# Kernel optimization log

Measured on AMD Instinct MI355X. Metric: run time of the kernel, lower is better.

## Reference

```python
import jax, jax.numpy as jnp
import numpy as np

B, P, E, D, A = 128, 196, 2048, 512, 512


def setup_inputs() -> dict:
    key = jax.random.key(0)
    ks = jax.random.split(key, 8)
    s = lambda fan_in: 1.0 / np.sqrt(fan_in)
    return {
        "encoder_out": jax.random.normal(ks[0], (B, P, E), jnp.float32),
        "decoder_hidden": jax.random.normal(ks[1], (B, D), jnp.float32),
        "We": jax.random.uniform(ks[2], (E, A), jnp.float32, -s(E), s(E)),
        "be": jax.random.uniform(ks[3], (A,), jnp.float32, -s(E), s(E)),
        "Wd": jax.random.uniform(ks[4], (D, A), jnp.float32, -s(D), s(D)),
        "bd": jax.random.uniform(ks[5], (A,), jnp.float32, -s(D), s(D)),
        "Wf": jax.random.uniform(ks[6], (A, 1), jnp.float32, -s(A), s(A)),
        "bf": jax.random.uniform(ks[7], (1,), jnp.float32, -s(A), s(A)),
    }


def reference(encoder_out, decoder_hidden, We, be, Wd, bd, Wf, bf):
    # att1: [B, P, A]
    att1 = jnp.einsum("bpe,ea->bpa", encoder_out, We) + be
    # att2: [B, A]
    att2 = decoder_hidden @ Wd + bd
    # additive attention scores: [B, P]
    att = (jax.nn.relu(att1 + att2[:, None, :]) @ Wf + bf)[..., 0]
    alpha = jax.nn.softmax(att, axis=1)  # softmax over pixels
    # weighted sum over pixels: [B, E]
    awe = jnp.einsum("bpe,bp->be", encoder_out, alpha)
    return awe, alpha
```

## Files before the change

kernel.cpp:

```cpp
#include <hip/hip_runtime.h>
#include <hip/hip_bf16.h>

typedef __attribute__((ext_vector_type(4))) float f32x4;
typedef __attribute__((ext_vector_type(4))) unsigned int u32x4;
typedef __attribute__((ext_vector_type(8))) short s16x8;

#define B_  128
#define P_  196
#define E_  2048
#define D_  512
#define A_  512
#define M_  (B_*P_)

typedef __attribute__((address_space(1))) const unsigned int gu32;
typedef __attribute__((address_space(3))) unsigned int lu32;
__device__ __forceinline__ void gl_lds16(const void* g, void* l) {
  __builtin_amdgcn_global_load_lds((gu32*)g, (lu32*)l, 16, 0, 0);
}

#define WAIT_VM6() asm volatile("s_waitcnt vmcnt(6)" ::: "memory")
#define WAIT_VM0() asm volatile("s_waitcnt vmcnt(0)" ::: "memory")
#define WAIT_LGKM0() asm volatile("s_waitcnt lgkmcnt(0)" ::: "memory")

__global__ void we_conv_kernel(const float* __restrict__ We,
                               unsigned short* __restrict__ WeTs) {
  __shared__ float tile[32][33];
  const int tx = threadIdx.x, ty = threadIdx.y;
  const int a0 = blockIdx.x * 32, e0 = blockIdx.y * 32;
  tile[ty][tx] = We[(e0 + ty) * A_ + a0 + tx];
  __syncthreads();
  const float v = tile[tx][ty];
  const unsigned int u = __float_as_uint(v);
  const unsigned short r = (unsigned short)((u + 0x7fffu + ((u >> 16) & 1u)) >> 16);
  const int a = a0 + ty;
  const int kt = blockIdx.y;
  const int c8 = tx >> 3, j = tx & 7;
  const int dest = ((a * 32 + c8 * 8) ^ ((a & 7) << 3)) + j;
  WeTs[kt * 16384 + dest] = r;
}

__global__ void att2_kernel(const float* __restrict__ h, const float* __restrict__ Wd,
                            const float* __restrict__ bd, const float* __restrict__ be,
                            float* __restrict__ att2pb) {
  const int b = blockIdx.x;
  const int t = threadIdx.x;
  __shared__ float hs[D_];
  hs[t] = h[b * D_ + t];
  hs[t + 256] = h[b * D_ + t + 256];
  __syncthreads();
  float a0 = 0.f, a1 = 0.f;
  for (int d = 0; d < D_; ++d) {
    const float hv = hs[d];
    a0 = fmaf(hv, Wd[d * A_ + t], a0);
    a1 = fmaf(hv, Wd[d * A_ + t + 256], a1);
  }
  att2pb[b * A_ + t] = a0 + bd[t] + be[t];
  att2pb[b * A_ + t + 256] = a1 + bd[t + 256] + be[t + 256];
}

__device__ inline unsigned pk2(float a, float b) {
  union { __hip_bfloat162 h; unsigned u; } cv;
  cv.h = __float22bfloat162_rn(make_float2(a, b));
  return cv.u;
}
__device__ inline u32x4 cvt8(const f32x4 lo, const f32x4 hi) {
  u32x4 r;
  r[0] = pk2(lo[0], lo[1]);
  r[1] = pk2(lo[2], lo[3]);
  r[2] = pk2(hi[0], hi[1]);
  r[3] = pk2(hi[2], hi[3]);
  return r;
}

__launch_bounds__(512, 2)
__global__ void score_kernel(const float* __restrict__ enc,
                             const unsigned short* __restrict__ WeTs,
                             const float* __restrict__ att2pb,
                             const float* __restrict__ Wf,
                             float* __restrict__ att_part) {
  __shared__ unsigned short Bh[3][512 * 32];
  __shared__ unsigned short Ahs[3][128 * 32];

  const int bid = blockIdx.x;
  const int m0 = bid * 128;

  const int t = threadIdx.x;
  const int lane = t & 63, w = t >> 6;
  const int wm = (w >> 2) * 64;
  const int wn = (w & 3) * 128;

  const int ar = t >> 2, ac = t & 3;
  const float* aptr = enc + (size_t)(m0 + ar) * E_ + ac * 8;
  const int awz = (ar * 32 + ac * 8) ^ ((ar & 7) << 3);
  const int doff = t * 8;

  const int q = lane >> 4, fr = lane & 15;
  const int fx = (fr & 7) << 3;
  int fa[4], fb[8];
#pragma unroll
  for (int i = 0; i < 4; ++i) fa[i] = ((wm + i * 16 + fr) * 32 + q * 8) ^ fx;
#pragma unroll
  for (int j = 0; j < 8; ++j) fb[j] = ((wn + j * 16 + fr) * 32 + q * 8) ^ fx;

  const f32x4 zero = {0.f, 0.f, 0.f, 0.f};
  f32x4 acc[4][8];
#pragma unroll
  for (int mi = 0; mi < 4; ++mi)
#pragma unroll
    for (int ni = 0; ni < 8; ++ni) acc[mi][ni] = zero;

  unsigned short *bAc = &Ahs[0][0], *bA1 = &Ahs[1][0], *bA2 = &Ahs[2][0];
  unsigned short *bBc = &Bh[0][0],  *bB1 = &Bh[1][0],  *bB2 = &Bh[2][0];

  f32x4 aC0, aC1, aN0, aN1;

  {
    aC0 = *(const f32x4*)(aptr);
    aC1 = *(const f32x4*)(aptr + 4);
#pragma unroll
    for (int i = 0; i < 4; ++i)
      gl_lds16(WeTs + i * 4096 + doff, bBc + i * 4096 + doff);
    aN0 = *(const f32x4*)(aptr + 32);
    aN1 = *(const f32x4*)(aptr + 36);
#pragma unroll
    for (int i = 0; i < 4; ++i)
      gl_lds16(WeTs + 16384 + i * 4096 + doff, bB1 + i * 4096 + doff);
    const u32x4 av = cvt8(aC0, aC1);
    *(u32x4*)(bAc + awz) = av;
    aC0 = aN0; aC1 = aN1;
    WAIT_VM6();
    WAIT_LGKM0();
    __builtin_amdgcn_s_barrier();
  }

  for (int it = 0; it < 62; ++it) {
    const int kof = (it + 2) * 32;
    aN0 = *(const f32x4*)(aptr + kof);
    aN1 = *(const f32x4*)(aptr + kof + 4);
    const unsigned short* srcB = WeTs + (size_t)(it + 2) * 16384;
#pragma unroll
    for (int i = 0; i < 4; ++i)
      gl_lds16(srcB + i * 4096 + doff, bB2 + i * 4096 + doff);

    s16x8 fah[4], fbh[8];
#pragma unroll
    for (int j = 0; j < 8; ++j) fbh[j] = *(const s16x8*)(bBc + fb[j]);
#pragma unroll
    for (int i = 0; i < 4; ++i) fah[i] = *(const s16x8*)(bAc + fa[i]);
    __builtin_amdgcn_s_setprio(1);
#pragma unroll
    for (int mi = 0; mi < 4; ++mi)
#pragma unroll
      for (int ni = 0; ni < 8; ++ni)
        acc[mi][ni] = __builtin_amdgcn_mfma_f32_16x16x32_bf16(fah[mi], fbh[ni], acc[mi][ni], 0, 0, 0);
    __builtin_amdgcn_s_setprio(0);

    {
      const u32x4 av = cvt8(aC0, aC1);
      *(u32x4*)(bA1 + awz) = av;
    }
    aC0 = aN0; aC1 = aN1;

    WAIT_VM6();
    WAIT_LGKM0();
    __builtin_amdgcn_s_barrier();

    unsigned short* tmp;
    tmp = bAc; bAc = bA1; bA1 = bA2; bA2 = tmp;
    tmp = bBc; bBc = bB1; bB1 = bB2; bB2 = tmp;
  }

  {
    s16x8 fah[4], fbh[8];
#pragma unroll
    for (int j = 0; j < 8; ++j) fbh[j] = *(const s16x8*)(bBc + fb[j]);
#pragma unroll
    for (int i = 0; i < 4; ++i) fah[i] = *(const s16x8*)(bAc + fa[i]);
    __builtin_amdgcn_s_setprio(1);
#pragma unroll
    for (int mi = 0; mi < 4; ++mi)
#pragma unroll
      for (int ni = 0; ni < 8; ++ni)
        acc[mi][ni] = __builtin_amdgcn_mfma_f32_16x16x32_bf16(fah[mi], fbh[ni], acc[mi][ni], 0, 0, 0);
    __builtin_amdgcn_s_setprio(0);
    const u32x4 av = cvt8(aC0, aC1);
    *(u32x4*)(bA1 + awz) = av;
    WAIT_VM0();
    WAIT_LGKM0();
    __builtin_amdgcn_s_barrier();
  }

  {
    s16x8 fah[4], fbh[8];
#pragma unroll
    for (int j = 0; j < 8; ++j) fbh[j] = *(const s16x8*)(bB1 + fb[j]);
#pragma unroll
    for (int i = 0; i < 4; ++i) fah[i] = *(const s16x8*)(bA1 + fa[i]);
#pragma unroll
    for (int mi = 0; mi < 4; ++mi)
#pragma unroll
      for (int ni = 0; ni < 8; ++ni)
        acc[mi][ni] = __builtin_amdgcn_mfma_f32_16x16x32_bf16(fah[mi], fbh[ni], acc[mi][ni], 0, 0, 0);
  }

  const int colL = wn + fr;
  float wfv[8];
#pragma unroll
  for (int ni = 0; ni < 8; ++ni) wfv[ni] = Wf[colL + ni * 16];
#pragma unroll
  for (int mi = 0; mi < 4; ++mi) {
    const int rowb = m0 + wm + mi * 16 + (q << 2);
#pragma unroll
    for (int r = 0; r < 4; ++r) {
      const int row = rowb + r;
      const int bb = row / P_;
      const float* a2 = att2pb + bb * A_ + colL;
      float s = 0.f;
#pragma unroll
      for (int ni = 0; ni < 8; ++ni)
        s += fmaxf(acc[mi][ni][r] + a2[ni * 16], 0.f) * wfv[ni];
#pragma unroll
      for (int off = 1; off < 16; off <<= 1) s += __shfl_xor(s, off);
      if (fr == 0) att_part[row * 4 + (w & 3)] = s;
    }
  }
}

__global__ void softmax_awe_kernel(const float* __restrict__ enc,
                                   const float* __restrict__ att_part,
                                   float* __restrict__ out) {
  const int bid = blockIdx.x;
  const int b = bid >> 1, ch = bid & 1;
  const int t = threadIdx.x;
  __shared__ float sm[256];
  __shared__ float alpha_s[P_];

  float av = -1e30f;
  if (t < P_) {
    const float* apt = att_part + (b * P_ + t) * 4;
    av = (apt[0] + apt[1]) + (apt[2] + apt[3]);
  }
  sm[t] = av;
  __syncthreads();
  for (int st = 128; st > 0; st >>= 1) {
    if (t < st) sm[t] = fmaxf(sm[t], sm[t + st]);
    __syncthreads();
  }
  const float mx = sm[0];
  __syncthreads();
  float ev = 0.f;
  if (t < P_) ev = __expf(av - mx);
  sm[t] = ev;
  __syncthreads();
  for (int st = 128; st > 0; st >>= 1) {
    if (t < st) sm[t] += sm[t + st];
    __syncthreads();
  }
  const float denom = sm[0];
  const float al = ev / denom;
  if (t < P_) {
    alpha_s[t] = al;
    if (ch == 0) out[B_ * E_ + b * P_ + t] = al;
  }
  __syncthreads();

  const int e0 = ch * 1024 + t * 4;
  const float* ebase = enc + (size_t)b * P_ * E_ + e0;
  f32x4 acc = {0.f, 0.f, 0.f, 0.f};
  for (int p = 0; p < P_; ++p) {
    const f32x4 v = *(const f32x4*)(ebase + (size_t)p * E_);
    const float a = alpha_s[p];
    acc.x += a * v.x; acc.y += a * v.y; acc.z += a * v.z; acc.w += a * v.w;
  }
  *(f32x4*)(out + b * E_ + e0) = acc;
}

extern "C" void kernel_launch(void* const* d_in, const int* in_sizes, int n_in,
                              void* d_out, int out_size, void* d_ws, size_t ws_size,
                              hipStream_t stream) {
  const float* enc = (const float*)d_in[0];
  const float* h   = (const float*)d_in[1];
  const float* We  = (const float*)d_in[2];
  const float* be  = (const float*)d_in[3];
  const float* Wd  = (const float*)d_in[4];
  const float* bd  = (const float*)d_in[5];
  const float* Wf  = (const float*)d_in[6];
  float* out = (float*)d_out;

  float* att2pb = (float*)d_ws;
  float* att_part = att2pb + B_ * A_;
  unsigned short* WeTs = (unsigned short*)(att_part + M_ * 4);

  we_conv_kernel<<<dim3(A_ / 32, E_ / 32), dim3(32, 32), 0, stream>>>(We, WeTs);
  att2_kernel<<<B_, 256, 0, stream>>>(h, Wd, bd, be, att2pb);
  score_kernel<<<M_ / 128, 512, 0, stream>>>(enc, WeTs, att2pb, Wf, att_part);
  softmax_awe_kernel<<<B_ * 2, 256, 0, stream>>>(enc, att_part, out);
}
```

Before: 133.7 us.

## Split score GEMM N dimension into 128-wide tiles with XCD-aware block remap

The score GEMM changes from 128x512 tiles on 512-thread blocks to 128x128 tiles on 256-thread blocks. This gives four times as many blocks and smaller LDS and accumulator use per block, with three blocks per CU. The block index is remapped so that consecutive blocks on the same XCD share M rows, meant to improve L2 reuse of the encoder rows. The cost is that each encoder tile is loaded and converted to bf16 four times instead of once, and the attention partial sums widen to eight per row, which the softmax kernel must now reduce. The weight pre-layout is adjusted to match the per-N-block tiles.

```diff
diff --git a/kernel.cpp b/kernel.cpp
--- a/kernel.cpp
+++ b/kernel.cpp
@@ -34,9 +34,10 @@
   const unsigned short r = (unsigned short)((u + 0x7fffu + ((u >> 16) & 1u)) >> 16);
   const int a = a0 + ty;
   const int kt = blockIdx.y;
+  const int nb = a >> 7, al = a & 127;
   const int c8 = tx >> 3, j = tx & 7;
-  const int dest = ((a * 32 + c8 * 8) ^ ((a & 7) << 3)) + j;
-  WeTs[kt * 16384 + dest] = r;
+  const int dest = ((al * 32 + c8 * 8) ^ ((al & 7) << 3)) + j;
+  WeTs[(kt * 4 + nb) * 4096 + dest] = r;
 }
 
 __global__ void att2_kernel(const float* __restrict__ h, const float* __restrict__ Wd,
@@ -72,62 +73,72 @@
   return r;
 }
 
-__launch_bounds__(512, 2)
+__launch_bounds__(256, 3)
 __global__ void score_kernel(const float* __restrict__ enc,
                              const unsigned short* __restrict__ WeTs,
                              const float* __restrict__ att2pb,
                              const float* __restrict__ Wf,
                              float* __restrict__ att_part) {
-  __shared__ unsigned short Bh[3][512 * 32];
-  __shared__ unsigned short Ahs[3][128 * 32];
-
-  const int bid = blockIdx.x;
-  const int m0 = bid * 128;
+  __shared__ unsigned short Ahs[3][4096];
+  __shared__ unsigned short Bhs[3][4096];
+
+  const int orig = blockIdx.x;
+  const int bid = (orig & 7) * 98 + (orig >> 3);
+  const int mb = bid >> 2, nb = bid & 3;
+  const int m0 = mb * 128;
+  const int n0 = nb * 128;
 
   const int t = threadIdx.x;
   const int lane = t & 63, w = t >> 6;
-  const int wm = (w >> 2) * 64;
-  const int wn = (w & 3) * 128;
+  const int wm = (w >> 1) * 64;
+  const int wn = (w & 1) * 64;
 
   const int ar = t >> 2, ac = t & 3;
   const float* aptr = enc + (size_t)(m0 + ar) * E_ + ac * 8;
-  const int awz = (ar * 32 + ac * 8) ^ ((ar & 7) << 3);
+  const int awz0 = (ar * 32 + ac * 8) ^ ((ar & 7) << 3);
+  const int awz1 = ((ar + 64) * 32 + ac * 8) ^ ((ar & 7) << 3);
+
+  const unsigned short* bsrc = WeTs + (size_t)nb * 4096;
   const int doff = t * 8;
 
   const int q = lane >> 4, fr = lane & 15;
   const int fx = (fr & 7) << 3;
-  int fa[4], fb[8];
-#pragma unroll
-  for (int i = 0; i < 4; ++i) fa[i] = ((wm + i * 16 + fr) * 32 + q * 8) ^ fx;
-#pragma unroll
-  for (int j = 0; j < 8; ++j) fb[j] = ((wn + j * 16 + fr) * 32 + q * 8) ^ fx;
+  int fa[4], fb[4];
+#pragma unroll
+  for (int i = 0; i < 4; ++i) {
+    fa[i] = ((wm + i * 16 + fr) * 32 + q * 8) ^ fx;
+    fb[i] = ((wn + i * 16 + fr) * 32 + q * 8) ^ fx;
+  }
 
   const f32x4 zero = {0.f, 0.f, 0.f, 0.f};
-  f32x4 acc[4][8];
+  f32x4 acc[4][4];
 #pragma unroll
   for (int mi = 0; mi < 4; ++mi)
 #pragma unroll
-    for (int ni = 0; ni < 8; ++ni) acc[mi][ni] = zero;
+    for (int ni = 0; ni < 4; ++ni) acc[mi][ni] = zero;
 
   unsigned short *bAc = &Ahs[0][0], *bA1 = &Ahs[1][0], *bA2 = &Ahs[2][0];
-  unsigned short *bBc = &Bh[0][0],  *bB1 = &Bh[1][0],  *bB2 = &Bh[2][0];
-
-  f32x4 aC0, aC1, aN0, aN1;
+  unsigned short *bBc = &Bhs[0][0], *bB1 = &Bhs[1][0], *bB2 = &Bhs[2][0];
+
+  f32x4 aC[4], aN[4];
 
   {
-    aC0 = *(const f32x4*)(aptr);
-    aC1 = *(const f32x4*)(aptr + 4);
-#pragma unroll
-    for (int i = 0; i < 4; ++i)
-      gl_lds16(WeTs + i * 4096 + doff, bBc + i * 4096 + doff);
-    aN0 = *(const f32x4*)(aptr + 32);
-    aN1 = *(const f32x4*)(aptr + 36);
-#pragma unroll
-    for (int i = 0; i < 4; ++i)
-      gl_lds16(WeTs + 16384 + i * 4096 + doff, bB1 + i * 4096 + doff);
-    const u32x4 av = cvt8(aC0, aC1);
-    *(u32x4*)(bAc + awz) = av;
-    aC0 = aN0; aC1 = aN1;
+    aC[0] = *(const f32x4*)(aptr);
+    aC[1] = *(const f32x4*)(aptr + 4);
+    aC[2] = *(const f32x4*)(aptr + 64 * E_);
+    aC[3] = *(const f32x4*)(aptr + 64 * E_ + 4);
+    gl_lds16(bsrc + doff, bBc + doff);
+    gl_lds16(bsrc + 2048 + doff, bBc + 2048 + doff);
+    aN[0] = *(const f32x4*)(aptr + 32);
+    aN[1] = *(const f32x4*)(aptr + 36);
+    aN[2] = *(const f32x4*)(aptr + 64 * E_ + 32);
+    aN[3] = *(const f32x4*)(aptr + 64 * E_ + 36);
+    gl_lds16(bsrc + 16384 + doff, bB1 + doff);
+    gl_lds16(bsrc + 16384 + 2048 + doff, bB1 + 2048 + doff);
+    *(u32x4*)(bAc + awz0) = cvt8(aC[0], aC[1]);
+    *(u32x4*)(bAc + awz1) = cvt8(aC[2], aC[3]);
+#pragma unroll
+    for (int i = 0; i < 4; ++i) aC[i] = aN[i];
     WAIT_VM6();
     WAIT_LGKM0();
     __builtin_amdgcn_s_barrier();
@@ -135,31 +146,32 @@
 
   for (int it = 0; it < 62; ++it) {
     const int kof = (it + 2) * 32;
-    aN0 = *(const f32x4*)(aptr + kof);
-    aN1 = *(const f32x4*)(aptr + kof + 4);
-    const unsigned short* srcB = WeTs + (size_t)(it + 2) * 16384;
-#pragma unroll
-    for (int i = 0; i < 4; ++i)
-      gl_lds16(srcB + i * 4096 + doff, bB2 + i * 4096 + doff);
-
-    s16x8 fah[4], fbh[8];
-#pragma unroll
-    for (int j = 0; j < 8; ++j) fbh[j] = *(const s16x8*)(bBc + fb[j]);
-#pragma unroll
-    for (int i = 0; i < 4; ++i) fah[i] = *(const s16x8*)(bAc + fa[i]);
+    aN[0] = *(const f32x4*)(aptr + kof);
+    aN[1] = *(const f32x4*)(aptr + kof + 4);
+    aN[2] = *(const f32x4*)(aptr + kof + 64 * E_);
+    aN[3] = *(const f32x4*)(aptr + kof + 64 * E_ + 4);
+    const unsigned short* sb = bsrc + (size_t)(it + 2) * 16384;
+    gl_lds16(sb + doff, bB2 + doff);
+    gl_lds16(sb + 2048 + doff, bB2 + 2048 + doff);
+
+    s16x8 fah[4], fbh[4];
+#pragma unroll
+    for (int i = 0; i < 4; ++i) {
+      fah[i] = *(const s16x8*)(bAc + fa[i]);
+      fbh[i] = *(const s16x8*)(bBc + fb[i]);
+    }
     __builtin_amdgcn_s_setprio(1);
 #pragma unroll
     for (int mi = 0; mi < 4; ++mi)
 #pragma unroll
-      for (int ni = 0; ni < 8; ++ni)
+      for (int ni = 0; ni < 4; ++ni)
         acc[mi][ni] = __builtin_amdgcn_mfma_f32_16x16x32_bf16(fah[mi], fbh[ni], acc[mi][ni], 0, 0, 0);
     __builtin_amdgcn_s_setprio(0);
 
-    {
-      const u32x4 av = cvt8(aC0, aC1);
-      *(u32x4*)(bA1 + awz) = av;
-    }
-    aC0 = aN0; aC1 = aN1;
+    *(u32x4*)(bA1 + awz0) = cvt8(aC[0], aC[1]);
+    *(u32x4*)(bA1 + awz1) = cvt8(aC[2], aC[3]);
+#pragma unroll
+    for (int i = 0; i < 4; ++i) aC[i] = aN[i];
 
     WAIT_VM6();
     WAIT_LGKM0();
@@ -171,42 +183,44 @@
   }
 
   {
-    s16x8 fah[4], fbh[8];
-#pragma unroll
-    for (int j = 0; j < 8; ++j) fbh[j] = *(const s16x8*)(bBc + fb[j]);
-#pragma unroll
-    for (int i = 0; i < 4; ++i) fah[i] = *(const s16x8*)(bAc + fa[i]);
+    s16x8 fah[4], fbh[4];
+#pragma unroll
+    for (int i = 0; i < 4; ++i) {
+      fah[i] = *(const s16x8*)(bAc + fa[i]);
+      fbh[i] = *(const s16x8*)(bBc + fb[i]);
+    }
     __builtin_amdgcn_s_setprio(1);
 #pragma unroll
     for (int mi = 0; mi < 4; ++mi)
 #pragma unroll
-      for (int ni = 0; ni < 8; ++ni)
+      for (int ni = 0; ni < 4; ++ni)
         acc[mi][ni] = __builtin_amdgcn_mfma_f32_16x16x32_bf16(fah[mi], fbh[ni], acc[mi][ni], 0, 0, 0);
     __builtin_amdgcn_s_setprio(0);
-    const u32x4 av = cvt8(aC0, aC1);
-    *(u32x4*)(bA1 + awz) = av;
+    *(u32x4*)(bA1 + awz0) = cvt8(aC[0], aC[1]);
+    *(u32x4*)(bA1 + awz1) = cvt8(aC[2], aC[3]);
     WAIT_VM0();
     WAIT_LGKM0();
     __builtin_amdgcn_s_barrier();
   }
 
   {
-    s16x8 fah[4], fbh[8];
-#pragma unroll
-    for (int j = 0; j < 8; ++j) fbh[j] = *(const s16x8*)(bB1 + fb[j]);
-#pragma unroll
-    for (int i = 0; i < 4; ++i) fah[i] = *(const s16x8*)(bA1 + fa[i]);
+    s16x8 fah[4], fbh[4];
+#pragma unroll
+    for (int i = 0; i < 4; ++i) {
+      fah[i] = *(const s16x8*)(bA1 + fa[i]);
+      fbh[i] = *(const s16x8*)(bB1 + fb[i]);
+    }
 #pragma unroll
     for (int mi = 0; mi < 4; ++mi)
 #pragma unroll
-      for (int ni = 0; ni < 8; ++ni)
+      for (int ni = 0; ni < 4; ++ni)
         acc[mi][ni] = __builtin_amdgcn_mfma_f32_16x16x32_bf16(fah[mi], fbh[ni], acc[mi][ni], 0, 0, 0);
   }
 
-  const int colL = wn + fr;
-  float wfv[8];
-#pragma unroll
-  for (int ni = 0; ni < 8; ++ni) wfv[ni] = Wf[colL + ni * 16];
+  const int colL = n0 + wn + fr;
+  float wfv[4];
+#pragma unroll
+  for (int ni = 0; ni < 4; ++ni) wfv[ni] = Wf[colL + ni * 16];
 #pragma unroll
   for (int mi = 0; mi < 4; ++mi) {
     const int rowb = m0 + wm + mi * 16 + (q << 2);
@@ -217,11 +231,11 @@
       const float* a2 = att2pb + bb * A_ + colL;
       float s = 0.f;
 #pragma unroll
-      for (int ni = 0; ni < 8; ++ni)
+      for (int ni = 0; ni < 4; ++ni)
         s += fmaxf(acc[mi][ni][r] + a2[ni * 16], 0.f) * wfv[ni];
 #pragma unroll
       for (int off = 1; off < 16; off <<= 1) s += __shfl_xor(s, off);
-      if (fr == 0) att_part[row * 4 + (w & 3)] = s;
+      if (fr == 0) att_part[row * 8 + nb * 2 + (w & 1)] = s;
     }
   }
 }
@@ -237,8 +251,11 @@
 
   float av = -1e30f;
   if (t < P_) {
-    const float* apt = att_part + (b * P_ + t) * 4;
-    av = (apt[0] + apt[1]) + (apt[2] + apt[3]);
+    const float* apt = att_part + (b * P_ + t) * 8;
+    float s = 0.f;
+#pragma unroll
+    for (int i = 0; i < 8; ++i) s += apt[i];
+    av = s;
   }
   sm[t] = av;
   __syncthreads();
@@ -289,10 +306,10 @@
 
   float* att2pb = (float*)d_ws;
   float* att_part = att2pb + B_ * A_;
-  unsigned short* WeTs = (unsigned short*)(att_part + M_ * 4);
+  unsigned short* WeTs = (unsigned short*)(att_part + M_ * 8);
 
   we_conv_kernel<<<dim3(A_ / 32, E_ / 32), dim3(32, 32), 0, stream>>>(We, WeTs);
   att2_kernel<<<B_, 256, 0, stream>>>(h, Wd, bd, be, att2pb);
-  score_kernel<<<M_ / 128, 512, 0, stream>>>(enc, WeTs, att2pb, Wf, att_part);
+  score_kernel<<<(M_ / 128) * 4, 256, 0, stream>>>(enc, WeTs, att2pb, Wf, att_part);
   softmax_awe_kernel<<<B_ * 2, 256, 0, stream>>>(enc, att_part, out);
 }
```

Measured after the change: 160.9 us. +20.3%, slower.

## Load encoder A fragments directly into registers, bypassing LDS staging

Applied to the files above, without the earlier changes.

The fp32 encoder tile is no longer converted and written into a shared-memory A buffer. Each wave now loads its own MFMA A-fragment rows straight from global memory into registers and converts them to bf16 there. The A LDS buffers, the LDS stores and the A fragment reads are removed, and the vmcnt waits are retuned for the new load counts. In exchange, the four column-group waves that share the same rows each load those rows themselves, which raises global and L2 traffic fourfold for A and uses more registers for eight prefetched vectors.

```diff
diff --git a/kernel.cpp b/kernel.cpp
--- a/kernel.cpp
+++ b/kernel.cpp
@@ -18,8 +18,9 @@
   __builtin_amdgcn_global_load_lds((gu32*)g, (lu32*)l, 16, 0, 0);
 }
 
-#define WAIT_VM6() asm volatile("s_waitcnt vmcnt(6)" ::: "memory")
-#define WAIT_VM0() asm volatile("s_waitcnt vmcnt(0)" ::: "memory")
+#define WAIT_VM4()  asm volatile("s_waitcnt vmcnt(4)"  ::: "memory")
+#define WAIT_VM8()  asm volatile("s_waitcnt vmcnt(8)"  ::: "memory")
+#define WAIT_VM12() asm volatile("s_waitcnt vmcnt(12)" ::: "memory")
 #define WAIT_LGKM0() asm volatile("s_waitcnt lgkmcnt(0)" ::: "memory")
 
 __global__ void we_conv_kernel(const float* __restrict__ We,
@@ -63,13 +64,13 @@
   cv.h = __float22bfloat162_rn(make_float2(a, b));
   return cv.u;
 }
-__device__ inline u32x4 cvt8(const f32x4 lo, const f32x4 hi) {
-  u32x4 r;
-  r[0] = pk2(lo[0], lo[1]);
-  r[1] = pk2(lo[2], lo[3]);
-  r[2] = pk2(hi[0], hi[1]);
-  r[3] = pk2(hi[2], hi[3]);
-  return r;
+__device__ inline s16x8 cvt8s(const f32x4 lo, const f32x4 hi) {
+  union { u32x4 u; s16x8 s; } c;
+  c.u[0] = pk2(lo[0], lo[1]);
+  c.u[1] = pk2(lo[2], lo[3]);
+  c.u[2] = pk2(hi[0], hi[1]);
+  c.u[3] = pk2(hi[2], hi[3]);
+  return c.s;
 }
 
 __launch_bounds__(512, 2)
@@ -78,8 +79,7 @@
                              const float* __restrict__ att2pb,
                              const float* __restrict__ Wf,
                              float* __restrict__ att_part) {
-  __shared__ unsigned short Bh[3][512 * 32];
-  __shared__ unsigned short Ahs[3][128 * 32];
+  __shared__ unsigned short Bhs[3][16384];
 
   const int bid = blockIdx.x;
   const int m0 = bid * 128;
@@ -89,16 +89,14 @@
   const int wm = (w >> 2) * 64;
   const int wn = (w & 3) * 128;
 
-  const int ar = t >> 2, ac = t & 3;
-  const float* aptr = enc + (size_t)(m0 + ar) * E_ + ac * 8;
-  const int awz = (ar * 32 + ac * 8) ^ ((ar & 7) << 3);
+  const int q = lane >> 4, fr = lane & 15;
+
+  const float* afr = enc + (size_t)(m0 + wm + fr) * E_ + q * 8;
+
   const int doff = t * 8;
 
-  const int q = lane >> 4, fr = lane & 15;
   const int fx = (fr & 7) << 3;
-  int fa[4], fb[8];
-#pragma unroll
-  for (int i = 0; i < 4; ++i) fa[i] = ((wm + i * 16 + fr) * 32 + q * 8) ^ fx;
+  int fb[8];
 #pragma unroll
   for (int j = 0; j < 8; ++j) fb[j] = ((wn + j * 16 + fr) * 32 + q * 8) ^ fx;
 
@@ -109,44 +107,75 @@
 #pragma unroll
     for (int ni = 0; ni < 8; ++ni) acc[mi][ni] = zero;
 
-  unsigned short *bAc = &Ahs[0][0], *bA1 = &Ahs[1][0], *bA2 = &Ahs[2][0];
-  unsigned short *bBc = &Bh[0][0],  *bB1 = &Bh[1][0],  *bB2 = &Bh[2][0];
-
-  f32x4 aC0, aC1, aN0, aN1;
+  unsigned short *bBc = &Bhs[0][0], *bB1 = &Bhs[1][0], *bB2 = &Bhs[2][0];
+
+  f32x4 aC[8];
 
   {
-    aC0 = *(const f32x4*)(aptr);
-    aC1 = *(const f32x4*)(aptr + 4);
+#pragma unroll
+    for (int i = 0; i < 4; ++i) {
+      aC[2 * i]     = *(const f32x4*)(afr + (size_t)i * 16 * E_);
+      aC[2 * i + 1] = *(const f32x4*)(afr + (size_t)i * 16 * E_ + 4);
+    }
 #pragma unroll
     for (int i = 0; i < 4; ++i)
       gl_lds16(WeTs + i * 4096 + doff, bBc + i * 4096 + doff);
-    aN0 = *(const f32x4*)(aptr + 32);
-    aN1 = *(const f32x4*)(aptr + 36);
 #pragma unroll
     for (int i = 0; i < 4; ++i)
       gl_lds16(WeTs + 16384 + i * 4096 + doff, bB1 + i * 4096 + doff);
-    const u32x4 av = cvt8(aC0, aC1);
-    *(u32x4*)(bAc + awz) = av;
-    aC0 = aN0; aC1 = aN1;
-    WAIT_VM6();
+    WAIT_VM4();
+    __builtin_amdgcn_s_barrier();
+  }
+
+  for (int it = 0; it < 62; ++it) {
+    s16x8 fah[4];
+#pragma unroll
+    for (int i = 0; i < 4; ++i) fah[i] = cvt8s(aC[2 * i], aC[2 * i + 1]);
+
+    {
+      const int kof = (it + 1) * 32;
+#pragma unroll
+      for (int i = 0; i < 4; ++i) {
+        aC[2 * i]     = *(const f32x4*)(afr + (size_t)i * 16 * E_ + kof);
+        aC[2 * i + 1] = *(const f32x4*)(afr + (size_t)i * 16 * E_ + kof + 4);
+      }
+      const unsigned short* sb = WeTs + (size_t)(it + 2) * 16384;
+#pragma unroll
+      for (int i = 0; i < 4; ++i)
+        gl_lds16(sb + i * 4096 + doff, bB2 + i * 4096 + doff);
+    }
+
+    s16x8 fbh[8];
+#pragma unroll
+    for (int j = 0; j < 8; ++j) fbh[j] = *(const s16x8*)(bBc + fb[j]);
+    __builtin_amdgcn_s_setprio(1);
+#pragma unroll
+    for (int mi = 0; mi < 4; ++mi)
+#pragma unroll
+      for (int ni = 0; ni < 8; ++ni)
+        acc[mi][ni] = __builtin_amdgcn_mfma_f32_16x16x32_bf16(fah[mi], fbh[ni], acc[mi][ni], 0, 0, 0);
+    __builtin_amdgcn_s_setprio(0);
+
+    WAIT_VM12();
     WAIT_LGKM0();
     __builtin_amdgcn_s_barrier();
-  }
-
-  for (int it = 0; it < 62; ++it) {
-    const int kof = (it + 2) * 32;
-    aN0 = *(const f32x4*)(aptr + kof);
-    aN1 = *(const f32x4*)(aptr + kof + 4);
-    const unsigned short* srcB = WeTs + (size_t)(it + 2) * 16384;
-#pragma unroll
-    for (int i = 0; i < 4; ++i)
-      gl_lds16(srcB + i * 4096 + doff, bB2 + i * 4096 + doff);
-
-    s16x8 fah[4], fbh[8];
+
+    unsigned short* tmp = bBc; bBc = bB1; bB1 = bB2; bB2 = tmp;
+  }
+
+  {
+    s16x8 fah[4];
+#pragma unroll
+    for (int i = 0; i < 4; ++i) fah[i] = cvt8s(aC[2 * i], aC[2 * i + 1]);
+    const int kof = 63 * 32;
+#pragma unroll
+    for (int i = 0; i < 4; ++i) {
+      aC[2 * i]     = *(const f32x4*)(afr + (size_t)i * 16 * E_ + kof);
+      aC[2 * i + 1] = *(const f32x4*)(afr + (size_t)i * 16 * E_ + kof + 4);
+    }
+    s16x8 fbh[8];
 #pragma unroll
     for (int j = 0; j < 8; ++j) fbh[j] = *(const s16x8*)(bBc + fb[j]);
-#pragma unroll
-    for (int i = 0; i < 4; ++i) fah[i] = *(const s16x8*)(bAc + fa[i]);
     __builtin_amdgcn_s_setprio(1);
 #pragma unroll
     for (int mi = 0; mi < 4; ++mi)
@@ -154,48 +183,19 @@
       for (int ni = 0; ni < 8; ++ni)
         acc[mi][ni] = __builtin_amdgcn_mfma_f32_16x16x32_bf16(fah[mi], fbh[ni], acc[mi][ni], 0, 0, 0);
     __builtin_amdgcn_s_setprio(0);
-
-    {
-      const u32x4 av = cvt8(aC0, aC1);
-      *(u32x4*)(bA1 + awz) = av;
-    }
-    aC0 = aN0; aC1 = aN1;
-
-    WAIT_VM6();
+    WAIT_VM8();
     WAIT_LGKM0();
     __builtin_amdgcn_s_barrier();
-
-    unsigned short* tmp;
-    tmp = bAc; bAc = bA1; bA1 = bA2; bA2 = tmp;
-    tmp = bBc; bBc = bB1; bB1 = bB2; bB2 = tmp;
+    unsigned short* tmp = bBc; bBc = bB1; bB1 = bB2; bB2 = tmp;
   }
 
   {
-    s16x8 fah[4], fbh[8];
+    s16x8 fah[4];
+#pragma unroll
+    for (int i = 0; i < 4; ++i) fah[i] = cvt8s(aC[2 * i], aC[2 * i + 1]);
+    s16x8 fbh[8];
 #pragma unroll
     for (int j = 0; j < 8; ++j) fbh[j] = *(const s16x8*)(bBc + fb[j]);
-#pragma unroll
-    for (int i = 0; i < 4; ++i) fah[i] = *(const s16x8*)(bAc + fa[i]);
-    __builtin_amdgcn_s_setprio(1);
-#pragma unroll
-    for (int mi = 0; mi < 4; ++mi)
-#pragma unroll
-      for (int ni = 0; ni < 8; ++ni)
-        acc[mi][ni] = __builtin_amdgcn_mfma_f32_16x16x32_bf16(fah[mi], fbh[ni], acc[mi][ni], 0, 0, 0);
-    __builtin_amdgcn_s_setprio(0);
-    const u32x4 av = cvt8(aC0, aC1);
-    *(u32x4*)(bA1 + awz) = av;
-    WAIT_VM0();
-    WAIT_LGKM0();
-    __builtin_amdgcn_s_barrier();
-  }
-
-  {
-    s16x8 fah[4], fbh[8];
-#pragma unroll
-    for (int j = 0; j < 8; ++j) fbh[j] = *(const s16x8*)(bB1 + fb[j]);
-#pragma unroll
-    for (int i = 0; i < 4; ++i) fah[i] = *(const s16x8*)(bA1 + fa[i]);
 #pragma unroll
     for (int mi = 0; mi < 4; ++mi)
 #pragma unroll
```

Measured after the change: 200.2 us. 1.5x slower.

## Split GEMM main loop into four barrier-separated phases interleaving loads and MFMAs

Applied to the files above, without the earlier changes.

Restructures each K-iteration of the att1 GEMM into four phases. Each phase issues a slice of LDS fragment reads and one async global-to-LDS copy, then runs a block of 8 MFMAs, with extra barriers between phases. This aims to keep the loads interleaved with matrix work and to align waves so memory and compute overlap, similar to ping-pong scheduling. In exchange it adds seven block barriers per iteration, which can stall waves if they are not balanced.

```diff
diff --git a/kernel.cpp b/kernel.cpp
--- a/kernel.cpp
+++ b/kernel.cpp
@@ -134,35 +134,76 @@
   }
 
   for (int it = 0; it < 62; ++it) {
+    const unsigned short* sb = WeTs + (size_t)(it + 2) * 16384;
     const int kof = (it + 2) * 32;
+    s16x8 fah[4], fbh[8];
+
+    fah[0] = *(const s16x8*)(bAc + fa[0]);
+    fah[1] = *(const s16x8*)(bAc + fa[1]);
+    fah[2] = *(const s16x8*)(bAc + fa[2]);
+    fah[3] = *(const s16x8*)(bAc + fa[3]);
+    fbh[0] = *(const s16x8*)(bBc + fb[0]);
+    fbh[1] = *(const s16x8*)(bBc + fb[1]);
+    gl_lds16(sb + doff, bB2 + doff);
     aN0 = *(const f32x4*)(aptr + kof);
     aN1 = *(const f32x4*)(aptr + kof + 4);
-    const unsigned short* srcB = WeTs + (size_t)(it + 2) * 16384;
-#pragma unroll
-    for (int i = 0; i < 4; ++i)
-      gl_lds16(srcB + i * 4096 + doff, bB2 + i * 4096 + doff);
-
-    s16x8 fah[4], fbh[8];
-#pragma unroll
-    for (int j = 0; j < 8; ++j) fbh[j] = *(const s16x8*)(bBc + fb[j]);
-#pragma unroll
-    for (int i = 0; i < 4; ++i) fah[i] = *(const s16x8*)(bAc + fa[i]);
-    __builtin_amdgcn_s_setprio(1);
-#pragma unroll
-    for (int mi = 0; mi < 4; ++mi)
-#pragma unroll
-      for (int ni = 0; ni < 8; ++ni)
-        acc[mi][ni] = __builtin_amdgcn_mfma_f32_16x16x32_bf16(fah[mi], fbh[ni], acc[mi][ni], 0, 0, 0);
-    __builtin_amdgcn_s_setprio(0);
-
+    __builtin_amdgcn_s_barrier();
+    WAIT_LGKM0();
+    __builtin_amdgcn_s_setprio(1);
+#pragma unroll
+    for (int mi = 0; mi < 4; ++mi) {
+      acc[mi][0] = __builtin_amdgcn_mfma_f32_16x16x32_bf16(fah[mi], fbh[0], acc[mi][0], 0, 0, 0);
+      acc[mi][1] = __builtin_amdgcn_mfma_f32_16x16x32_bf16(fah[mi], fbh[1], acc[mi][1], 0, 0, 0);
+    }
+    __builtin_amdgcn_s_setprio(0);
+    __builtin_amdgcn_s_barrier();
+
+    fbh[2] = *(const s16x8*)(bBc + fb[2]);
+    fbh[3] = *(const s16x8*)(bBc + fb[3]);
+    gl_lds16(sb + 4096 + doff, bB2 + 4096 + doff);
+    __builtin_amdgcn_s_barrier();
+    WAIT_LGKM0();
+    __builtin_amdgcn_s_setprio(1);
+#pragma unroll
+    for (int mi = 0; mi < 4; ++mi) {
+      acc[mi][2] = __builtin_amdgcn_mfma_f32_16x16x32_bf16(fah[mi], fbh[2], acc[mi][2], 0, 0, 0);
+      acc[mi][3] = __builtin_amdgcn_mfma_f32_16x16x32_bf16(fah[mi], fbh[3], acc[mi][3], 0, 0, 0);
+    }
+    __builtin_amdgcn_s_setprio(0);
+    __builtin_amdgcn_s_barrier();
+
+    fbh[4] = *(const s16x8*)(bBc + fb[4]);
+    fbh[5] = *(const s16x8*)(bBc + fb[5]);
+    gl_lds16(sb + 8192 + doff, bB2 + 8192 + doff);
+    __builtin_amdgcn_s_barrier();
+    WAIT_LGKM0();
+    __builtin_amdgcn_s_setprio(1);
+#pragma unroll
+    for (int mi = 0; mi < 4; ++mi) {
+      acc[mi][4] = __builtin_amdgcn_mfma_f32_16x16x32_bf16(fah[mi], fbh[4], acc[mi][4], 0, 0, 0);
+      acc[mi][5] = __builtin_amdgcn_mfma_f32_16x16x32_bf16(fah[mi], fbh[5], acc[mi][5], 0, 0, 0);
+    }
+    __builtin_amdgcn_s_setprio(0);
+    __builtin_amdgcn_s_barrier();
+
+    fbh[6] = *(const s16x8*)(bBc + fb[6]);
+    fbh[7] = *(const s16x8*)(bBc + fb[7]);
+    gl_lds16(sb + 12288 + doff, bB2 + 12288 + doff);
     {
       const u32x4 av = cvt8(aC0, aC1);
       *(u32x4*)(bA1 + awz) = av;
     }
     aC0 = aN0; aC1 = aN1;
-
+    __builtin_amdgcn_s_barrier();
+    WAIT_LGKM0();
+    __builtin_amdgcn_s_setprio(1);
+#pragma unroll
+    for (int mi = 0; mi < 4; ++mi) {
+      acc[mi][6] = __builtin_amdgcn_mfma_f32_16x16x32_bf16(fah[mi], fbh[6], acc[mi][6], 0, 0, 0);
+      acc[mi][7] = __builtin_amdgcn_mfma_f32_16x16x32_bf16(fah[mi], fbh[7], acc[mi][7], 0, 0, 0);
+    }
+    __builtin_amdgcn_s_setprio(0);
     WAIT_VM6();
-    WAIT_LGKM0();
     __builtin_amdgcn_s_barrier();
 
     unsigned short* tmp;
```

Result: slower. 139.2 us (+4.1%).
